# Kernel tuning notes

Measured on AMD Instinct MI355X. Metric: run time of the kernel, lower is better.

Reference implementation:

```python
import jax, jax.numpy as jnp
import numpy as np


def setup_inputs() -> dict:
    key = jax.random.key(0)
    k1, k2, k3 = jax.random.split(key, 3)
    B, C, H, Wd = 32, 768, 32, 32
    K, DQ = 64, 16
    features = jax.random.normal(k1, (B, C, H, Wd), dtype=jnp.float32)
    query = jax.random.normal(k2, (B, DQ, H, Wd), dtype=jnp.float32)
    # Ensemble of 1x1 convs (bias=False): weight [K, dim_query, dim]
    W = jax.random.normal(k3, (K, DQ, C), dtype=jnp.float32) * (1.0 / np.sqrt(C))
    return {"features": features, "query": query, "W": W}


def reference(features, query, W):
    # Ensemble 1x1 conv: key_values [K, B, DQ, H, W]
    kv = jnp.einsum('bchw,kqc->kbqhw', features, W)
    K, B = kv.shape[0], kv.shape[1]
    # cdist between query (b, 1, d) and keys (b, k, d), d = DQ*H*W
    q_flat = query.reshape(B, -1)                       # [B, D]
    k_flat = jnp.moveaxis(kv.reshape(K, B, -1), 0, 1)   # [B, K, D]
    diff = q_flat[:, None, :] - k_flat                  # [B, K, D]
    distance = jnp.sqrt(jnp.sum(diff * diff, axis=-1))  # [B, K]
    # logits = -distance; codes = argmax(logits) == argmin(distance)
    codes = jnp.argmin(distance, axis=-1)               # [B]
    # per-batch gather of selected key_values
    sel = kv[codes, jnp.arange(B)]                      # [B, DQ, H, W]
    commit_loss = jnp.mean((sel - query) ** 2)
    return sel, codes, commit_loss
```

## Files before the change

kernel.cpp:

```cpp
#include <hip/hip_runtime.h>
#include <cstdint>
#include <cstddef>

typedef float f4 __attribute__((ext_vector_type(4)));
typedef float f32x4 __attribute__((ext_vector_type(4)));
typedef short short8 __attribute__((ext_vector_type(8)));
typedef unsigned short u16x8 __attribute__((ext_vector_type(8)));
typedef unsigned short u16x4 __attribute__((ext_vector_type(4)));
typedef unsigned short ushort_t;

#define B_   32
#define C_   768
#define HW_  1024
#define DQ_  16
#define K_   64
#define M_   1024
#define NHWT 16
#define NCT  12

#define CODE_OFF 524288
#define LOSS_OFF 524320

__device__ __forceinline__ unsigned bf16_rne_bits(float x) {
    unsigned u = __builtin_bit_cast(unsigned, x);
    return (u + 0x7FFFu + ((u >> 16) & 1u)) >> 16;
}
__device__ __forceinline__ float bits_to_f32(unsigned hi16) {
    unsigned u = hi16 << 16;
    return __builtin_bit_cast(float, u);
}
__device__ __forceinline__ void split_bf16(float x, unsigned short& hi, unsigned short& lo) {
    unsigned h = bf16_rne_bits(x);
    hi = (unsigned short)h;
    float r = x - bits_to_f32(h);
    lo = (unsigned short)bf16_rne_bits(r);
}


__global__ __launch_bounds__(256)
void k0_splitF(const float* __restrict__ Fp,
               ushort_t* __restrict__ FhiT, ushort_t* __restrict__ FloT)
{
    __shared__ float tile[64][65];
    const int t = threadIdx.x;
    const int ht = blockIdx.x, ct = blockIdx.y, b = blockIdx.z;

#pragma unroll
    for (int rep = 0; rep < 4; ++rep) {
        int idx = rep * 256 + t;
        int c_l = idx >> 4;
        int hwf = (idx & 15) * 4;
        f4 v = *(const f4*)&Fp[((size_t)b * C_ + ct * 64 + c_l) * HW_ + ht * 64 + hwf];
        tile[c_l][hwf + 0] = v.x;
        tile[c_l][hwf + 1] = v.y;
        tile[c_l][hwf + 2] = v.z;
        tile[c_l][hwf + 3] = v.w;
    }
    __syncthreads();

#pragma unroll
    for (int rep = 0; rep < 2; ++rep) {
        int hw_l = (t >> 3) + rep * 32;
        int cg   = (t & 7) * 8;
        unsigned short hi[8], lo[8];
#pragma unroll
        for (int j = 0; j < 8; ++j)
            split_bf16(tile[cg + j][hw_l], hi[j], lo[j]);
        size_t o = (((size_t)(b * NCT + ct)) * HW_ + ht * 64 + hw_l) * 64 + cg;
        *(u16x8*)&FhiT[o] = *(u16x8*)hi;
        *(u16x8*)&FloT[o] = *(u16x8*)lo;
    }
}

__global__ __launch_bounds__(256)
void k0_splitW(const float* __restrict__ Wp,
               ushort_t* __restrict__ Whi, ushort_t* __restrict__ Wlo)
{
    const unsigned gid = blockIdx.x * 256 + threadIdx.x;
    const unsigned base = gid * 4;
    const unsigned m = base / C_;
    const unsigned c = base - m * C_;
    const unsigned ct = c >> 6, cl = c & 63;
    f4 v = *(const f4*)&Wp[base];
    unsigned short hi[4], lo[4];
    split_bf16(v.x, hi[0], lo[0]);
    split_bf16(v.y, hi[1], lo[1]);
    split_bf16(v.z, hi[2], lo[2]);
    split_bf16(v.w, hi[3], lo[3]);
    size_t o = ((size_t)ct * M_ + m) * 64 + cl;
    *(u16x4*)&Whi[o] = *(u16x4*)hi;
    *(u16x4*)&Wlo[o] = *(u16x4*)lo;
}

#define NKT 36

__global__ __launch_bounds__(512, 2)
void k1_mfma8(const ushort_t* __restrict__ Whi, const ushort_t* __restrict__ Wlo,
              const ushort_t* __restrict__ FhiT, const ushort_t* __restrict__ FloT,
              const float* __restrict__ Qp, float* __restrict__ partial)
{
    __shared__ ushort_t lds[2][32768];

    const int tid  = threadIdx.x;
    const int w    = tid >> 6;
    const int lane = tid & 63;

    const int bid = blockIdx.x;
    const int idx = (bid & 7) * 64 + (bid >> 3);
    const int mt  = idx & 3;
    const int hwt = (idx >> 2) & 3;
    const int b   = idx >> 4;

    const int wm = w >> 2, wn = w & 3;

    const bool isA    = (w < 4);
    const int  wrow0  = (w & 3) * 64;
    const int  srow   = lane >> 3;
    const int  sslot  = (lane & 7) ^ srow;
    const int  regoff = isA ? 0 : 16384;

    const int c15 = lane & 15, d0 = lane >> 4;
    int offA[8][2], offB[4][2];
#pragma unroll
    for (int i = 0; i < 8; ++i) {
        int m = wm * 128 + i * 16 + c15;
#pragma unroll
        for (int kh = 0; kh < 2; ++kh) {
            int d = kh * 4 + d0;
            offA[i][kh] = m * 64 + ((d ^ (m & 7)) << 3);
        }
    }
#pragma unroll
    for (int j = 0; j < 4; ++j) {
        int n = wn * 64 + j * 16 + c15;
#pragma unroll
        for (int kh = 0; kh < 2; ++kh) {
            int d = kh * 4 + d0;
            offB[j][kh] = 16384 + n * 64 + ((d ^ (n & 7)) << 3);
        }
    }

    f32x4 acc[8][4] = {};

    {
        const ushort_t* sb = isA ? (Whi + (size_t)(mt * 256) * 64)
                                 : (FhiT + ((size_t)(b * NCT) * HW_ + hwt * 256) * 64);
#pragma unroll
        for (int ii = 0; ii < 8; ++ii) {
            const ushort_t* g = sb + (size_t)(wrow0 + ii * 8 + srow) * 64 + sslot * 8;
            __builtin_amdgcn_global_load_lds(
                (const __attribute__((address_space(1))) void*)g,
                (__attribute__((address_space(3))) void*)&lds[0][regoff + (wrow0 + ii * 8) * 64],
                16, 0, 0);
        }
    }
    asm volatile("s_waitcnt vmcnt(0)" ::: "memory");
    __builtin_amdgcn_s_barrier();

    short8 af[4][2], bf0[2][2], bf1[2][2];

#define STAGE4(II)                                                                               \
    if (do_stage) {                                                                              \
        _Pragma("unroll")                                                                        \
        for (int ii = (II); ii < (II) + 4; ++ii) {                                               \
            const ushort_t* g = sb + (size_t)(wrow0 + ii * 8 + srow) * 64 + sslot * 8;           \
            __builtin_amdgcn_global_load_lds(                                                    \
                (const __attribute__((address_space(1))) void*)g,                                \
                (__attribute__((address_space(3))) void*)(Lnext + regoff + (wrow0 + ii * 8) * 64),\
                16, 0, 0);                                                                       \
        }                                                                                        \
    }

#define QUAD(I0, J0, BF)                                                                         \
    _Pragma("unroll")                                                                            \
    for (int i4 = 0; i4 < 4; ++i4)                                                               \
        _Pragma("unroll")                                                                        \
        for (int j2 = 0; j2 < 2; ++j2)                                                           \
            _Pragma("unroll")                                                                    \
            for (int kh = 0; kh < 2; ++kh)                                                       \
                acc[(I0) + i4][(J0) + j2] = __builtin_amdgcn_mfma_f32_16x16x32_bf16(             \
                    af[i4][kh], BF[j2][kh], acc[(I0) + i4][(J0) + j2], 0, 0, 0);

#define PRE_MFMA()                                          \
    __builtin_amdgcn_s_barrier();                           \
    asm volatile("s_waitcnt lgkmcnt(0)" ::: "memory");      \
    __builtin_amdgcn_sched_barrier(0);                      \
    __builtin_amdgcn_s_setprio(1);

#define POST_MFMA()                                         \
    __builtin_amdgcn_s_setprio(0);                          \
    __builtin_amdgcn_sched_barrier(0);                      \
    __builtin_amdgcn_s_barrier();

    for (int t = 0; t < NKT; ++t) {
        const int cur = t & 1;
        const ushort_t* L = &lds[cur][0];
        ushort_t* Lnext = &lds[cur ^ 1][0];

        const bool do_stage = (t + 1 < NKT);
        const int tt = do_stage ? (t + 1) : 0;
        const int term = (tt >= 24) ? 2 : ((tt >= 12) ? 1 : 0);
        const int ct = tt - term * 12;
        const ushort_t* sb;
        if (isA) sb = ((term == 1) ? Wlo : Whi) + ((size_t)ct * M_ + mt * 256) * 64;
        else     sb = ((term == 2) ? FloT : FhiT) + ((size_t)(b * NCT + ct) * HW_ + hwt * 256) * 64;

#pragma unroll
        for (int i4 = 0; i4 < 4; ++i4)
#pragma unroll
            for (int kh = 0; kh < 2; ++kh)
                af[i4][kh] = *(const short8*)&L[offA[i4][kh]];
#pragma unroll
        for (int j2 = 0; j2 < 2; ++j2)
#pragma unroll
            for (int kh = 0; kh < 2; ++kh)
                bf0[j2][kh] = *(const short8*)&L[offB[j2][kh]];
        STAGE4(0)
        PRE_MFMA()
        QUAD(0, 0, bf0)
        POST_MFMA()

#pragma unroll
        for (int j2 = 0; j2 < 2; ++j2)
#pragma unroll
            for (int kh = 0; kh < 2; ++kh)
                bf1[j2][kh] = *(const short8*)&L[offB[2 + j2][kh]];
        STAGE4(4)
        PRE_MFMA()
        QUAD(0, 2, bf1)
        POST_MFMA()

#pragma unroll
        for (int i4 = 0; i4 < 4; ++i4)
#pragma unroll
            for (int kh = 0; kh < 2; ++kh)
                af[i4][kh] = *(const short8*)&L[offA[4 + i4][kh]];
        PRE_MFMA()
        QUAD(4, 2, bf1)
        POST_MFMA()

        __builtin_amdgcn_s_barrier();
        __builtin_amdgcn_sched_barrier(0);
        __builtin_amdgcn_s_setprio(1);
        QUAD(4, 0, bf0)
        __builtin_amdgcn_s_setprio(0);
        __builtin_amdgcn_sched_barrier(0);
        asm volatile("s_waitcnt vmcnt(0)" ::: "memory");
        __builtin_amdgcn_s_barrier();
    }
#undef STAGE4
#undef QUAD
#undef PRE_MFMA
#undef POST_MFMA

    float qv[4][4];
#pragma unroll
    for (int j = 0; j < 4; ++j) {
        const int hw = hwt * 256 + wn * 64 + j * 16 + c15;
#pragma unroll
        for (int r = 0; r < 4; ++r)
            qv[j][r] = Qp[(size_t)(b * DQ_ + d0 * 4 + r) * HW_ + hw];
    }
#pragma unroll
    for (int i = 0; i < 8; ++i) {
        float s = 0.f;
#pragma unroll
        for (int j = 0; j < 4; ++j)
#pragma unroll
            for (int r = 0; r < 4; ++r) {
                float d = qv[j][r] - acc[i][j][r];
                s = fmaf(d, d, s);
            }
#pragma unroll
        for (int off = 32; off; off >>= 1) s += __shfl_xor(s, off);
        if (lane == 0) {
            const int k = mt * 16 + wm * 8 + i;
            partial[((size_t)b * K_ + k) * NHWT + hwt * 4 + wn] = s;
        }
    }
}

__global__ __launch_bounds__(1024)
void k2_select(const float* __restrict__ partial, float* __restrict__ out,
               int* __restrict__ codes_ws)
{
    const int tid = threadIdx.x;
    const int b = tid >> 5, kk = tid & 31;
    float s0 = 0.f, s1 = 0.f;
#pragma unroll
    for (int h = 0; h < NHWT; ++h) {
        s0 += partial[((size_t)b * K_ + kk) * NHWT + h];
        s1 += partial[((size_t)b * K_ + kk + 32) * NHWT + h];
    }
    float bv = s0; int bk = kk;
    if (s1 < bv) { bv = s1; bk = kk + 32; }
#pragma unroll
    for (int m = 16; m >= 1; m >>= 1) {
        float ov = __shfl_xor(bv, m);
        int   ok = __shfl_xor(bk, m);
        if (ov < bv || (ov == bv && ok < bk)) { bv = ov; bk = ok; }
    }
    __shared__ float mins[32];
    if (kk == 0) {
        out[CODE_OFF + b] = (float)bk;
        codes_ws[b] = bk;
        mins[b] = bv;
    }
    __syncthreads();
    if (tid == 0) {
        float t = 0.f;
#pragma unroll
        for (int i = 0; i < 32; ++i) t += mins[i];
        out[LOSS_OFF] = t * (1.0f / 524288.0f);
    }
}

__global__ __launch_bounds__(256)
void k3_mfma(const ushort_t* __restrict__ Whi, const ushort_t* __restrict__ Wlo,
             const ushort_t* __restrict__ FhiT, const ushort_t* __restrict__ FloT,
             const int* __restrict__ codes_ws, float* __restrict__ out)
{
    __shared__ ushort_t lds3[2][10240];

    const int tid = threadIdx.x;
    const int w = tid >> 6, lane = tid & 63;
    const int b = blockIdx.x >> 4, hwt = blockIdx.x & 15;
    const int code = codes_ws[b];

    const int srow = lane >> 3, sslot = (lane & 7) ^ srow;
    const int c15 = lane & 15, d0 = lane >> 4;

    int offAhi[2], offAlo[2], offBh[2], offBl[2];
#pragma unroll
    for (int kh = 0; kh < 2; ++kh) {
        const int d = kh * 4 + d0;
        const int mA = c15;
        offAhi[kh] = mA * 64 + ((d ^ (mA & 7)) << 3);
        const int mAl = 16 + c15;
        offAlo[kh] = mAl * 64 + ((d ^ (mAl & 7)) << 3);
        const int rB = w * 16 + c15;
        offBh[kh] = 2048 + rB * 64 + ((d ^ (rB & 7)) << 3);
        offBl[kh] = 6144 + rB * 64 + ((d ^ (rB & 7)) << 3);
    }

#define K3_STAGE(CT, BUF)                                                                        \
    {                                                                                            \
        ushort_t* Lb = &lds3[(BUF)][0];                                                          \
        const ushort_t* bhp = FhiT + ((size_t)(b * NCT + (CT)) * HW_ + hwt * 64) * 64;           \
        const ushort_t* blp = FloT + ((size_t)(b * NCT + (CT)) * HW_ + hwt * 64) * 64;           \
        _Pragma("unroll")                                                                        \
        for (int ii = 0; ii < 2; ++ii) {                                                         \
            __builtin_amdgcn_global_load_lds(                                                    \
                (const __attribute__((address_space(1))) void*)(bhp + (w * 16 + ii * 8 + srow) * 64 + sslot * 8), \
                (__attribute__((address_space(3))) void*)(Lb + 2048 + (w * 16 + ii * 8) * 64),   \
                16, 0, 0);                                                                       \
            __builtin_amdgcn_global_load_lds(                                                    \
                (const __attribute__((address_space(1))) void*)(blp + (w * 16 + ii * 8 + srow) * 64 + sslot * 8), \
                (__attribute__((address_space(3))) void*)(Lb + 6144 + (w * 16 + ii * 8) * 64),   \
                16, 0, 0);                                                                       \
        }                                                                                        \
        if (w == 0) {                                                                            \
            const ushort_t* ahp = Whi + ((size_t)(CT) * M_ + code * 16) * 64;                    \
            _Pragma("unroll")                                                                    \
            for (int ii = 0; ii < 2; ++ii)                                                       \
                __builtin_amdgcn_global_load_lds(                                                \
                    (const __attribute__((address_space(1))) void*)(ahp + (ii * 8 + srow) * 64 + sslot * 8), \
                    (__attribute__((address_space(3))) void*)(Lb + (ii * 8) * 64),               \
                    16, 0, 0);                                                                   \
        } else if (w == 1) {                                                                     \
            const ushort_t* alp = Wlo + ((size_t)(CT) * M_ + code * 16) * 64;                    \
            _Pragma("unroll")                                                                    \
            for (int ii = 0; ii < 2; ++ii)                                                       \
                __builtin_amdgcn_global_load_lds(                                                \
                    (const __attribute__((address_space(1))) void*)(alp + (ii * 8 + srow) * 64 + sslot * 8), \
                    (__attribute__((address_space(3))) void*)(Lb + (16 + ii * 8) * 64),          \
                    16, 0, 0);                                                                   \
        }                                                                                        \
    }

    f32x4 acc = {};

    K3_STAGE(0, 0)
    asm volatile("s_waitcnt vmcnt(0)" ::: "memory");
    __syncthreads();

    for (int ct = 0; ct < NCT; ++ct) {
        const int cur = ct & 1;
        if (ct + 1 < NCT) K3_STAGE(ct + 1, cur ^ 1)
        const ushort_t* L = &lds3[cur][0];
        short8 ah[2], al2[2], bh[2], bl[2];
#pragma unroll
        for (int kh = 0; kh < 2; ++kh) {
            ah[kh]  = *(const short8*)&L[offAhi[kh]];
            al2[kh] = *(const short8*)&L[offAlo[kh]];
            bh[kh]  = *(const short8*)&L[offBh[kh]];
            bl[kh]  = *(const short8*)&L[offBl[kh]];
        }
#pragma unroll
        for (int kh = 0; kh < 2; ++kh) {
            acc = __builtin_amdgcn_mfma_f32_16x16x32_bf16(ah[kh], bh[kh], acc, 0, 0, 0);
            acc = __builtin_amdgcn_mfma_f32_16x16x32_bf16(ah[kh], bl[kh], acc, 0, 0, 0);
            acc = __builtin_amdgcn_mfma_f32_16x16x32_bf16(al2[kh], bh[kh], acc, 0, 0, 0);
        }
        asm volatile("s_waitcnt vmcnt(0)" ::: "memory");
        __syncthreads();
    }
#undef K3_STAGE

#pragma unroll
    for (int r = 0; r < 4; ++r) {
        const int q = d0 * 4 + r;
        out[((size_t)(b * DQ_ + q)) * HW_ + hwt * 64 + w * 16 + c15] = acc[r];
    }
}

#define BM   256
#define BN   64
#define BC   32
#define NMT  4

__global__ __launch_bounds__(256)
void k1_dist_fp32(const float* __restrict__ Fp, const float* __restrict__ Qp,
                  const float* __restrict__ Wp, float* __restrict__ partial)
{
    __shared__ float w_lds[BC][BM];
    __shared__ float f_lds[BC][BN + 8];
    __shared__ float red[32][8];

    const int tid = threadIdx.x;
    const int mt = blockIdx.x, hwt = blockIdx.y, b = blockIdx.z;
    const int ty = tid >> 3, tx = tid & 7;
    const int m0 = ty * 8, hw0 = tx * 8;

    float acc[8][8];
#pragma unroll
    for (int i = 0; i < 8; ++i)
#pragma unroll
        for (int j = 0; j < 8; ++j) acc[i][j] = 0.f;

    for (int c0 = 0; c0 < C_; c0 += BC) {
#pragma unroll
        for (int i = 0; i < 8; ++i) {
            const int m_l = i * 32 + ty;
            const int c_l = tx * 4;
            const int col = m_l ^ (tx * 4);
            f4 w4 = *(const f4*)&Wp[(size_t)(mt * BM + m_l) * C_ + c0 + c_l];
            w_lds[c_l + 0][col] = w4.x;
            w_lds[c_l + 1][col] = w4.y;
            w_lds[c_l + 2][col] = w4.z;
            w_lds[c_l + 3][col] = w4.w;
        }
        {
            const int c = tid >> 3;
            const int hw = (tid & 7) * 8;
            const float* src = &Fp[((size_t)b * C_ + c0 + c) * HW_ + (size_t)hwt * BN + hw];
            *(f4*)&f_lds[c][hw]     = *(const f4*)src;
            *(f4*)&f_lds[c][hw + 4] = *(const f4*)(src + 4);
        }
        __syncthreads();

#pragma unroll 4
        for (int cc = 0; cc < BC; ++cc) {
            const int sw = ((cc >> 2) & 7) * 4;
            const int colA = m0 ^ sw;
            f4 w0 = *(const f4*)&w_lds[cc][colA];
            f4 w1 = *(const f4*)&w_lds[cc][colA ^ 4];
            f4 g0 = *(const f4*)&f_lds[cc][hw0];
            f4 g1 = *(const f4*)&f_lds[cc][hw0 + 4];
            const float wa[8] = {w0.x, w0.y, w0.z, w0.w, w1.x, w1.y, w1.z, w1.w};
            const float fv[8] = {g0.x, g0.y, g0.z, g0.w, g1.x, g1.y, g1.z, g1.w};
#pragma unroll
            for (int i = 0; i < 8; ++i)
#pragma unroll
                for (int j = 0; j < 8; ++j)
                    acc[i][j] = fmaf(wa[i], fv[j], acc[i][j]);
        }
        __syncthreads();
    }

    const int q0 = (ty & 1) * 8;
    float s = 0.f;
#pragma unroll
    for (int i = 0; i < 8; ++i) {
        const float* qp = &Qp[((size_t)b * DQ_ + q0 + i) * HW_ + (size_t)hwt * BN + hw0];
        f4 qa = *(const f4*)qp;
        f4 qb = *(const f4*)(qp + 4);
        float d;
        d = qa.x - acc[i][0]; s = fmaf(d, d, s);
        d = qa.y - acc[i][1]; s = fmaf(d, d, s);
        d = qa.z - acc[i][2]; s = fmaf(d, d, s);
        d = qa.w - acc[i][3]; s = fmaf(d, d, s);
        d = qb.x - acc[i][4]; s = fmaf(d, d, s);
        d = qb.y - acc[i][5]; s = fmaf(d, d, s);
        d = qb.z - acc[i][6]; s = fmaf(d, d, s);
        d = qb.w - acc[i][7]; s = fmaf(d, d, s);
    }
    red[ty][tx] = s;
    __syncthreads();
    if (tid < 16) {
        float t = 0.f;
#pragma unroll
        for (int r = 0; r < 2; ++r)
#pragma unroll
            for (int x = 0; x < 8; ++x) t += red[tid * 2 + r][x];
        partial[((size_t)b * K_ + mt * 16 + tid) * NHWT + hwt] = t;
    }
}

#define BN3 128
#define BC3 32

__global__ __launch_bounds__(256)
void k3_sel(const float* __restrict__ Fp, const float* __restrict__ Wp,
            const int* __restrict__ codes_ws, float* __restrict__ out)
{
    __shared__ float f_lds[BC3][BN3];
    __shared__ float w_lds[DQ_][33];

    const int tid = threadIdx.x;
    const int b = blockIdx.x >> 3, hwt = blockIdx.x & 7;
    const int code = codes_ws[b];
    const int q = tid >> 4;
    const int hw0 = (tid & 15) * 8;

    float a[8] = {0.f, 0.f, 0.f, 0.f, 0.f, 0.f, 0.f, 0.f};

    for (int c0 = 0; c0 < C_; c0 += BC3) {
        if (tid < 128) {
            const int qq = tid >> 3, c4 = (tid & 7) * 4;
            f4 w4 = *(const f4*)&Wp[((size_t)code * DQ_ + qq) * C_ + c0 + c4];
            w_lds[qq][c4 + 0] = w4.x;
            w_lds[qq][c4 + 1] = w4.y;
            w_lds[qq][c4 + 2] = w4.z;
            w_lds[qq][c4 + 3] = w4.w;
        }
        {
            const int c = tid >> 3;
            const int hw = (tid & 7) * 16;
            const float* src = &Fp[((size_t)b * C_ + c0 + c) * HW_ + (size_t)hwt * BN3 + hw];
            *(f4*)&f_lds[c][hw]      = *(const f4*)(src);
            *(f4*)&f_lds[c][hw + 4]  = *(const f4*)(src + 4);
            *(f4*)&f_lds[c][hw + 8]  = *(const f4*)(src + 8);
            *(f4*)&f_lds[c][hw + 12] = *(const f4*)(src + 12);
        }
        __syncthreads();
#pragma unroll 4
        for (int cc = 0; cc < BC3; ++cc) {
            const float wv = w_lds[q][cc];
            f4 g0 = *(const f4*)&f_lds[cc][hw0];
            f4 g1 = *(const f4*)&f_lds[cc][hw0 + 4];
            a[0] = fmaf(wv, g0.x, a[0]);
            a[1] = fmaf(wv, g0.y, a[1]);
            a[2] = fmaf(wv, g0.z, a[2]);
            a[3] = fmaf(wv, g0.w, a[3]);
            a[4] = fmaf(wv, g1.x, a[4]);
            a[5] = fmaf(wv, g1.y, a[5]);
            a[6] = fmaf(wv, g1.z, a[6]);
            a[7] = fmaf(wv, g1.w, a[7]);
        }
        __syncthreads();
    }

    float* dst = &out[((size_t)b * DQ_ + q) * HW_ + (size_t)hwt * BN3 + hw0];
    f4 o0 = {a[0], a[1], a[2], a[3]};
    f4 o1 = {a[4], a[5], a[6], a[7]};
    *(f4*)dst = o0;
    *(f4*)(dst + 4) = o1;
}

extern "C" void kernel_launch(void* const* d_in, const int* in_sizes, int n_in,
                              void* d_out, int out_size, void* d_ws, size_t ws_size,
                              hipStream_t stream)
{
    const float* Fp = (const float*)d_in[0];
    const float* Qp = (const float*)d_in[1];
    const float* Wp = (const float*)d_in[2];
    float* out = (float*)d_out;

    const size_t FT_ELEMS = (size_t)B_ * HW_ * C_;
    const size_t W_ELEMS  = (size_t)M_ * C_;
    const size_t PART_OFF = 4 * FT_ELEMS + 4 * W_ELEMS;
    const size_t CODE_WS  = PART_OFF + (size_t)B_ * K_ * NHWT * 4;
    const size_t NEED     = CODE_WS + 128;

    if (ws_size >= NEED) {
        ushort_t* FhiT = (ushort_t*)d_ws;
        ushort_t* FloT = FhiT + FT_ELEMS;
        ushort_t* Whi  = FloT + FT_ELEMS;
        ushort_t* Wlo  = Whi + W_ELEMS;
        float* partial = (float*)((char*)d_ws + PART_OFF);
        int* codes_ws  = (int*)((char*)d_ws + CODE_WS);

        k0_splitF<<<dim3(16, NCT, B_), 256, 0, stream>>>(Fp, FhiT, FloT);
        k0_splitW<<<dim3(W_ELEMS / 1024), 256, 0, stream>>>(Wp, Whi, Wlo);
        k1_mfma8<<<dim3(512), 512, 0, stream>>>(Whi, Wlo, FhiT, FloT, Qp, partial);
        k2_select<<<1, 1024, 0, stream>>>(partial, out, codes_ws);
        k3_mfma<<<dim3(B_ * 16), 256, 0, stream>>>(Whi, Wlo, FhiT, FloT, codes_ws, out);
    } else {
        float* partial = (float*)d_ws;
        int* codes_ws  = (int*)((char*)d_ws + (size_t)B_ * K_ * NHWT * 4);
        k1_dist_fp32<<<dim3(NMT, NHWT, B_), 256, 0, stream>>>(Fp, Qp, Wp, partial);
        k2_select<<<1, 1024, 0, stream>>>(partial, out, codes_ws);
        k3_sel<<<dim3(B_ * 8), 256, 0, stream>>>(Fp, Wp, codes_ws, out);
    }
}
```

Before: 309.6 us.

## Switch GEMM mainloop to 4-stage half-K pipeline with deeper prefetch

The main GEMM loop changes from a double-buffered 64-wide K tile to a 4-deep ring of 32-wide K half-tiles, with three stages prefetched ahead and a partial vmcnt wait instead of draining all loads each iteration. The LDS layout and swizzle are rewritten to pack two rows per 64-element line, and launch bounds drop to 1 block per CU. The aim is to hide global-to-LDS latency behind MFMA work. The cost is lower occupancy and more barriers per unit of K, and the wraparound prefetch at the end issues redundant loads.

```diff
diff --git a/kernel.cpp b/kernel.cpp
--- a/kernel.cpp
+++ b/kernel.cpp
@@ -17,6 +17,7 @@
 #define M_   1024
 #define NHWT 16
 #define NCT  12
+#define NHALF 72
 
 #define CODE_OFF 524288
 #define LOSS_OFF 524320
@@ -92,14 +93,12 @@
     *(u16x4*)&Wlo[o] = *(u16x4*)lo;
 }
 
-#define NKT 36
-
-__global__ __launch_bounds__(512, 2)
+__global__ __launch_bounds__(512, 1)
 void k1_mfma8(const ushort_t* __restrict__ Whi, const ushort_t* __restrict__ Wlo,
               const ushort_t* __restrict__ FhiT, const ushort_t* __restrict__ FloT,
               const float* __restrict__ Qp, float* __restrict__ partial)
 {
-    __shared__ ushort_t lds[2][32768];
+    __shared__ ushort_t lds[4][16384];
 
     const int tid  = threadIdx.x;
     const int w    = tid >> 6;
@@ -113,145 +112,102 @@
 
     const int wm = w >> 2, wn = w & 3;
 
-    const bool isA    = (w < 4);
-    const int  wrow0  = (w & 3) * 64;
-    const int  srow   = lane >> 3;
-    const int  sslot  = (lane & 7) ^ srow;
-    const int  regoff = isA ? 0 : 16384;
+    const bool isA   = (w < 4);
+    const int  wgrp  = w & 3;
+    const int  regoff = isA ? 0 : 8192;
+
+    const int q_l  = lane >> 3;
+    const int p_l  = lane & 7;
+    const int t_l  = p_l ^ (q_l & 7);
+    const int rloc_l = 2 * q_l + (t_l >> 2);
+    const int ks_l   = t_l & 3;
 
     const int c15 = lane & 15, d0 = lane >> 4;
-    int offA[8][2], offB[4][2];
+    int offA[8], offB[4];
 #pragma unroll
     for (int i = 0; i < 8; ++i) {
-        int m = wm * 128 + i * 16 + c15;
-#pragma unroll
-        for (int kh = 0; kh < 2; ++kh) {
-            int d = kh * 4 + d0;
-            offA[i][kh] = m * 64 + ((d ^ (m & 7)) << 3);
-        }
+        int r = wm * 128 + i * 16 + c15;
+        int q = r >> 1;
+        offA[i] = q * 64 + (((((r & 1) << 2) | d0) ^ (q & 7)) << 3);
     }
 #pragma unroll
     for (int j = 0; j < 4; ++j) {
-        int n = wn * 64 + j * 16 + c15;
-#pragma unroll
-        for (int kh = 0; kh < 2; ++kh) {
-            int d = kh * 4 + d0;
-            offB[j][kh] = 16384 + n * 64 + ((d ^ (n & 7)) << 3);
-        }
+        int r = wn * 64 + j * 16 + c15;
+        int q = r >> 1;
+        offB[j] = 8192 + q * 64 + (((((r & 1) << 2) | d0) ^ (q & 7)) << 3);
     }
 
     f32x4 acc[8][4] = {};
 
-    {
-        const ushort_t* sb = isA ? (Whi + (size_t)(mt * 256) * 64)
-                                 : (FhiT + ((size_t)(b * NCT) * HW_ + hwt * 256) * 64);
-#pragma unroll
-        for (int ii = 0; ii < 8; ++ii) {
-            const ushort_t* g = sb + (size_t)(wrow0 + ii * 8 + srow) * 64 + sslot * 8;
-            __builtin_amdgcn_global_load_lds(
-                (const __attribute__((address_space(1))) void*)g,
-                (__attribute__((address_space(3))) void*)&lds[0][regoff + (wrow0 + ii * 8) * 64],
-                16, 0, 0);
-        }
-    }
-    asm volatile("s_waitcnt vmcnt(0)" ::: "memory");
+#define STAGE_SETUP(GG)                                                                  \
+    const int stile = (GG) >> 1, shalf = (GG) & 1;                                       \
+    const int sterm = (stile >= 24) ? 2 : ((stile >= 12) ? 1 : 0);                       \
+    const int sct   = stile - sterm * 12;                                                \
+    const ushort_t* sb;                                                                  \
+    if (isA) sb = ((sterm == 1) ? Wlo : Whi) + ((size_t)sct * M_ + mt * 256) * 64;       \
+    else     sb = ((sterm == 2) ? FloT : FhiT) + ((size_t)(b * NCT + sct) * HW_ + hwt * 256) * 64; \
+    sb += shalf * 32 + (size_t)(wgrp * 64 + rloc_l) * 64 + ks_l * 8;                     \
+    ushort_t* Dst = &lds[(GG) & 3][regoff + wgrp * 2048];
+
+#define STAGE1(II)                                                                       \
+    __builtin_amdgcn_global_load_lds(                                                    \
+        (const __attribute__((address_space(1))) void*)(sb + (II) * 1024),               \
+        (__attribute__((address_space(3))) void*)(Dst + (II) * 512),                     \
+        16, 0, 0);
+
+#pragma unroll
+    for (int h = 0; h < 3; ++h) {
+        STAGE_SETUP(h)
+        STAGE1(0) STAGE1(1) STAGE1(2) STAGE1(3)
+    }
+    asm volatile("s_waitcnt vmcnt(8)" ::: "memory");
     __builtin_amdgcn_s_barrier();
 
-    short8 af[4][2], bf0[2][2], bf1[2][2];
-
-#define STAGE4(II)                                                                               \
-    if (do_stage) {                                                                              \
-        _Pragma("unroll")                                                                        \
-        for (int ii = (II); ii < (II) + 4; ++ii) {                                               \
-            const ushort_t* g = sb + (size_t)(wrow0 + ii * 8 + srow) * 64 + sslot * 8;           \
-            __builtin_amdgcn_global_load_lds(                                                    \
-                (const __attribute__((address_space(1))) void*)g,                                \
-                (__attribute__((address_space(3))) void*)(Lnext + regoff + (wrow0 + ii * 8) * 64),\
-                16, 0, 0);                                                                       \
-        }                                                                                        \
-    }
-
-#define QUAD(I0, J0, BF)                                                                         \
-    _Pragma("unroll")                                                                            \
-    for (int i4 = 0; i4 < 4; ++i4)                                                               \
-        _Pragma("unroll")                                                                        \
-        for (int j2 = 0; j2 < 2; ++j2)                                                           \
-            _Pragma("unroll")                                                                    \
-            for (int kh = 0; kh < 2; ++kh)                                                       \
-                acc[(I0) + i4][(J0) + j2] = __builtin_amdgcn_mfma_f32_16x16x32_bf16(             \
-                    af[i4][kh], BF[j2][kh], acc[(I0) + i4][(J0) + j2], 0, 0, 0);
-
-#define PRE_MFMA()                                          \
-    __builtin_amdgcn_s_barrier();                           \
-    asm volatile("s_waitcnt lgkmcnt(0)" ::: "memory");      \
-    __builtin_amdgcn_sched_barrier(0);                      \
-    __builtin_amdgcn_s_setprio(1);
-
-#define POST_MFMA()                                         \
-    __builtin_amdgcn_s_setprio(0);                          \
-    __builtin_amdgcn_sched_barrier(0);                      \
-    __builtin_amdgcn_s_barrier();
-
-    for (int t = 0; t < NKT; ++t) {
-        const int cur = t & 1;
-        const ushort_t* L = &lds[cur][0];
-        ushort_t* Lnext = &lds[cur ^ 1][0];
-
-        const bool do_stage = (t + 1 < NKT);
-        const int tt = do_stage ? (t + 1) : 0;
-        const int term = (tt >= 24) ? 2 : ((tt >= 12) ? 1 : 0);
-        const int ct = tt - term * 12;
-        const ushort_t* sb;
-        if (isA) sb = ((term == 1) ? Wlo : Whi) + ((size_t)ct * M_ + mt * 256) * 64;
-        else     sb = ((term == 2) ? FloT : FhiT) + ((size_t)(b * NCT + ct) * HW_ + hwt * 256) * 64;
-
-#pragma unroll
-        for (int i4 = 0; i4 < 4; ++i4)
-#pragma unroll
-            for (int kh = 0; kh < 2; ++kh)
-                af[i4][kh] = *(const short8*)&L[offA[i4][kh]];
-#pragma unroll
-        for (int j2 = 0; j2 < 2; ++j2)
-#pragma unroll
-            for (int kh = 0; kh < 2; ++kh)
-                bf0[j2][kh] = *(const short8*)&L[offB[j2][kh]];
-        STAGE4(0)
-        PRE_MFMA()
-        QUAD(0, 0, bf0)
-        POST_MFMA()
-
-#pragma unroll
-        for (int j2 = 0; j2 < 2; ++j2)
-#pragma unroll
-            for (int kh = 0; kh < 2; ++kh)
-                bf1[j2][kh] = *(const short8*)&L[offB[2 + j2][kh]];
-        STAGE4(4)
-        PRE_MFMA()
-        QUAD(0, 2, bf1)
-        POST_MFMA()
-
-#pragma unroll
-        for (int i4 = 0; i4 < 4; ++i4)
-#pragma unroll
-            for (int kh = 0; kh < 2; ++kh)
-                af[i4][kh] = *(const short8*)&L[offA[4 + i4][kh]];
-        PRE_MFMA()
-        QUAD(4, 2, bf1)
-        POST_MFMA()
-
+    short8 af[4], bf[4];
+
+    for (int g = 0; g < NHALF; ++g) {
+        const ushort_t* L = &lds[g & 3][0];
+        const int ggw = g + 3;
+        const int gg  = (ggw >= NHALF) ? ggw - NHALF : ggw;
+        STAGE_SETUP(gg)
+
+#pragma unroll
+        for (int i = 0; i < 4; ++i) af[i] = *(const short8*)&L[offA[i]];
+#pragma unroll
+        for (int j = 0; j < 4; ++j) bf[j] = *(const short8*)&L[offB[j]];
+        STAGE1(0) STAGE1(1)
         __builtin_amdgcn_s_barrier();
+        asm volatile("s_waitcnt lgkmcnt(0)" ::: "memory");
         __builtin_amdgcn_sched_barrier(0);
         __builtin_amdgcn_s_setprio(1);
-        QUAD(4, 0, bf0)
+#pragma unroll
+        for (int i = 0; i < 4; ++i)
+#pragma unroll
+            for (int j = 0; j < 4; ++j)
+                acc[i][j] = __builtin_amdgcn_mfma_f32_16x16x32_bf16(af[i], bf[j], acc[i][j], 0, 0, 0);
         __builtin_amdgcn_s_setprio(0);
         __builtin_amdgcn_sched_barrier(0);
-        asm volatile("s_waitcnt vmcnt(0)" ::: "memory");
         __builtin_amdgcn_s_barrier();
-    }
-#undef STAGE4
-#undef QUAD
-#undef PRE_MFMA
-#undef POST_MFMA
+
+#pragma unroll
+        for (int i = 0; i < 4; ++i) af[i] = *(const short8*)&L[offA[4 + i]];
+        STAGE1(2) STAGE1(3)
+        __builtin_amdgcn_s_barrier();
+        asm volatile("s_waitcnt lgkmcnt(0)" ::: "memory");
+        __builtin_amdgcn_sched_barrier(0);
+        __builtin_amdgcn_s_setprio(1);
+#pragma unroll
+        for (int i = 0; i < 4; ++i)
+#pragma unroll
+            for (int j = 0; j < 4; ++j)
+                acc[4 + i][j] = __builtin_amdgcn_mfma_f32_16x16x32_bf16(af[i], bf[j], acc[4 + i][j], 0, 0, 0);
+        __builtin_amdgcn_s_setprio(0);
+        __builtin_amdgcn_sched_barrier(0);
+        asm volatile("s_waitcnt vmcnt(8)" ::: "memory");
+        __builtin_amdgcn_s_barrier();
+    }
+#undef STAGE1
+#undef STAGE_SETUP
 
     float qv[4][4];
 #pragma unroll
```

After: 322.0 us. 1.04x slower.
